# Performance work log

Hardware: AMD Instinct MI355X
Metric: run time of the kernel (lower is better)

## Reference

```python
import jax, jax.numpy as jnp
import numpy as np

DIM = 1024
HEADS = 16
HEAD_DIM = DIM // HEADS
HIDDEN = 4 * DIM
EPS = 1e-5


def layernorm(x, g, b):
    mu = jnp.mean(x, axis=-1, keepdims=True)
    var = jnp.var(x, axis=-1, keepdims=True)
    return (x - mu) * jax.lax.rsqrt(var + EPS) * g + b


def setup_inputs() -> dict:
    key = jax.random.key(0)
    ks = jax.random.split(key, 6)
    B, N = 4, 1024
    s = lambda fan_in: 1.0 / np.sqrt(fan_in)
    return {
        "x": jax.random.normal(ks[0], (B, N, DIM), jnp.float32),
        "ln1_g": jnp.ones((DIM,), jnp.float32),
        "ln1_b": jnp.zeros((DIM,), jnp.float32),
        "qkv_w": jax.random.normal(ks[1], (3 * DIM, DIM), jnp.float32) * s(DIM),
        "qkv_b": jnp.zeros((3 * DIM,), jnp.float32),
        "proj_w": jax.random.normal(ks[2], (DIM, DIM), jnp.float32) * s(DIM),
        "proj_b": jnp.zeros((DIM,), jnp.float32),
        "ln2_g": jnp.ones((DIM,), jnp.float32),
        "ln2_b": jnp.zeros((DIM,), jnp.float32),
        "fc1_w": jax.random.normal(ks[3], (HIDDEN, DIM), jnp.float32) * s(DIM),
        "fc1_b": jnp.zeros((HIDDEN,), jnp.float32),
        "fc2_w": jax.random.normal(ks[4], (DIM, HIDDEN), jnp.float32) * s(HIDDEN),
        "fc2_b": jnp.zeros((DIM,), jnp.float32),
    }


def reference(x, ln1_g, ln1_b, qkv_w, qkv_b, proj_w, proj_b,
              ln2_g, ln2_b, fc1_w, fc1_b, fc2_w, fc2_b):
    B, N, C = x.shape
    scale = HEAD_DIM ** -0.5

    # --- attention branch ---
    h = layernorm(x, ln1_g, ln1_b)
    qkv = h @ qkv_w.T + qkv_b                      # [B,N,3C]
    qkv = qkv.reshape(B, N, 3, HEADS, HEAD_DIM)
    q = qkv[:, :, 0].transpose(0, 2, 1, 3) * scale  # [B,H,N,D]
    k = qkv[:, :, 1].transpose(0, 2, 1, 3)
    v = qkv[:, :, 2].transpose(0, 2, 1, 3)
    attn = jax.nn.softmax(jnp.einsum('bhnd,bhmd->bhnm', q, k), axis=-1)
    o = jnp.einsum('bhnm,bhmd->bhnd', attn, v)      # [B,H,N,D]
    o = o.transpose(0, 2, 1, 3).reshape(B, N, C)
    x = x + (o @ proj_w.T + proj_b)

    # --- mlp branch ---
    h = layernorm(x, ln2_g, ln2_b)
    h = jax.nn.gelu(h @ fc1_w.T + fc1_b, approximate=False)
    x = x + (h @ fc2_w.T + fc2_b)
    return x
```

## Files before the change

kernel.cpp:

```cpp
#include <hip/hip_runtime.h>
#include <math.h>

#define DIM 1024
#define HEADS 16
#define HEAD_DIM 64
#define HIDDEN 4096
#define NSEQ 1024
#define BATCH 4
#define TOKENS (BATCH * NSEQ)
#define EPS 1e-5f

typedef __bf16 bf16;
typedef __bf16 bf16x4 __attribute__((ext_vector_type(4)));
typedef __bf16 bf16x8 __attribute__((ext_vector_type(8)));
typedef float f32x4 __attribute__((ext_vector_type(4)));

#define AS1 __attribute__((address_space(1)))
#define AS3 __attribute__((address_space(3)))

__global__ __launch_bounds__(256) void cvt4_kernel(const float* __restrict__ s0,
                                                   const float* __restrict__ s1,
                                                   const float* __restrict__ s2,
                                                   const float* __restrict__ s3,
                                                   bf16* __restrict__ d0,
                                                   bf16* __restrict__ d1,
                                                   bf16* __restrict__ d2,
                                                   bf16* __restrict__ d3) {
    size_t q = (size_t)blockIdx.x * 256 + threadIdx.x;
    const float* s;
    bf16* d;
    if (q < 786432) { s = s0; d = d0; }
    else if (q < 786432 + 262144) { q -= 786432; s = s1; d = d1; }
    else if (q < 786432 + 262144 + 1048576) { q -= 786432 + 262144; s = s2; d = d2; }
    else { q -= 786432 + 262144 + 1048576; s = s3; d = d3; }
    const float4 v = *(const float4*)(s + q * 4);
    bf16x4 o = {(bf16)v.x, (bf16)v.y, (bf16)v.z, (bf16)v.w};
    *(bf16x4*)(d + q * 4) = o;
}

__global__ __launch_bounds__(256) void ln_kernel(const float* __restrict__ x,
                                                 const float* __restrict__ g,
                                                 const float* __restrict__ b,
                                                 bf16* __restrict__ out) {
    const int t = blockIdx.x;
    const int tid = threadIdx.x;
    const float* row = x + (size_t)t * DIM;
    float v[4];
    float s1 = 0.f, s2 = 0.f;
#pragma unroll
    for (int i = 0; i < 4; i++) {
        v[i] = row[tid + i * 256];
        s1 += v[i];
        s2 += v[i] * v[i];
    }
    __shared__ float w1[4], w2[4];
#pragma unroll
    for (int off = 32; off > 0; off >>= 1) {
        s1 += __shfl_down(s1, off, 64);
        s2 += __shfl_down(s2, off, 64);
    }
    const int wave = tid >> 6;
    if ((tid & 63) == 0) { w1[wave] = s1; w2[wave] = s2; }
    __syncthreads();
    const float sum = w1[0] + w1[1] + w1[2] + w1[3];
    const float ssq = w2[0] + w2[1] + w2[2] + w2[3];
    const float mu = sum * (1.0f / DIM);
    const float var = ssq * (1.0f / DIM) - mu * mu;
    const float rstd = rsqrtf(var + EPS);
    bf16* orow = out + (size_t)t * DIM;
#pragma unroll
    for (int i = 0; i < 4; i++) {
        const int idx = tid + i * 256;
        orow[idx] = (bf16)((v[i] - mu) * rstd * g[idx] + b[idx]);
    }
}

#define ACT_NONE 0
#define ACT_GELU 1

template <int ACT, bool RES, bool OUT_BF16, bool VT, int SPLITK>
__global__ __launch_bounds__(256) void mfma_gemm(const bf16* __restrict__ A,
                                                 const bf16* __restrict__ W,
                                                 const float* __restrict__ bias,
                                                 const float* __restrict__ res,
                                                 void* __restrict__ Cout,
                                                 bf16* __restrict__ vTout,
                                                 int M, int N, int K) {
    __shared__ __align__(16) bf16 As[128 * 32];
    __shared__ __align__(16) bf16 Bs[128 * 32];

    const int tid = threadIdx.x;
    const int w = tid >> 6, lane = tid & 63;
    const int bm = blockIdx.y * 128, bn = blockIdx.x * 128;
    const int kseg = K / SPLITK;
    const int k0 = (SPLITK > 1) ? blockIdx.z * kseg : 0;

    const bf16* pa = A + (size_t)(bm + (tid >> 2)) * K + k0 + (tid & 3) * 8;
    const bf16* pb = W + (size_t)(bn + (tid >> 2)) * K + k0 + (tid & 3) * 8;
    const size_t rowskip = (size_t)64 * K;
    char* ldsA = (char*)As + (w << 10);
    char* ldsB = (char*)Bs + (w << 10);

    const int wm = (w & 1) * 64, wn = (w >> 1) * 64;
    const int fm = lane & 15, fk = (lane >> 4) * 8;
    const bf16* aoff = As + (wm + fm) * 32 + fk;
    const bf16* boff = Bs + (wn + fm) * 32 + fk;

    f32x4 acc[4][4] = {};

    for (int kk = 0; kk < kseg; kk += 32) {
        __builtin_amdgcn_global_load_lds((const AS1 void*)pa, (AS3 void*)ldsA, 16, 0, 0);
        __builtin_amdgcn_global_load_lds((const AS1 void*)(pa + rowskip), (AS3 void*)(ldsA + 4096), 16, 0, 0);
        __builtin_amdgcn_global_load_lds((const AS1 void*)pb, (AS3 void*)ldsB, 16, 0, 0);
        __builtin_amdgcn_global_load_lds((const AS1 void*)(pb + rowskip), (AS3 void*)(ldsB + 4096), 16, 0, 0);
        pa += 32; pb += 32;
        __syncthreads();

        bf16x8 af[4], bfr[4];
#pragma unroll
        for (int t = 0; t < 4; t++) af[t] = *(const bf16x8*)(aoff + t * 16 * 32);
#pragma unroll
        for (int t = 0; t < 4; t++) bfr[t] = *(const bf16x8*)(boff + t * 16 * 32);
#pragma unroll
        for (int mt = 0; mt < 4; mt++)
#pragma unroll
            for (int nt = 0; nt < 4; nt++)
                acc[mt][nt] = __builtin_amdgcn_mfma_f32_16x16x32_bf16(af[mt], bfr[nt], acc[mt][nt], 0, 0, 0);
        __syncthreads();
    }

    const int cn = bn + wn + fm;
    const int rm = bm + wm + (lane >> 4) * 4;
    float bv[4];
#pragma unroll
    for (int nt = 0; nt < 4; nt++)
        bv[nt] = (SPLITK > 1 && blockIdx.z != 0) ? 0.f : bias[cn + nt * 16];

    if (SPLITK > 1) {
        float* outp = (float*)Cout;
#pragma unroll
        for (int mt = 0; mt < 4; mt++) {
#pragma unroll
            for (int r = 0; r < 4; r++) {
                const size_t rowoff = (size_t)(rm + mt * 16 + r) * N;
#pragma unroll
                for (int nt = 0; nt < 4; nt++)
                    atomicAdd(outp + rowoff + cn + nt * 16, acc[mt][nt][r] + bv[nt]);
            }
        }
        return;
    }

    if (VT && bn >= 2048) {
        const int dg0 = cn - 2048;
#pragma unroll
        for (int mt = 0; mt < 4; mt++) {
            const int mrow = rm + mt * 16;
            const int bI = mrow >> 10, j0 = mrow & 1023;
#pragma unroll
            for (int nt = 0; nt < 4; nt++) {
                const int dg = dg0 + nt * 16;
                bf16x4 v4 = {(bf16)(acc[mt][nt][0] + bv[nt]), (bf16)(acc[mt][nt][1] + bv[nt]),
                             (bf16)(acc[mt][nt][2] + bv[nt]), (bf16)(acc[mt][nt][3] + bv[nt])};
                *(bf16x4*)(vTout + ((size_t)(bI * 1024 + dg)) * 1024 + j0) = v4;
            }
        }
        return;
    }

#pragma unroll
    for (int mt = 0; mt < 4; mt++) {
#pragma unroll
        for (int r = 0; r < 4; r++) {
            const size_t rowoff = (size_t)(rm + mt * 16 + r) * N;
#pragma unroll
            for (int nt = 0; nt < 4; nt++) {
                float val = acc[mt][nt][r] + bv[nt];
                if (ACT == ACT_GELU) val = 0.5f * val * (1.0f + erff(val * 0.70710678118654752f));
                if (RES) val += res[rowoff + cn + nt * 16];
                if (OUT_BF16) ((bf16*)Cout)[rowoff + cn + nt * 16] = (bf16)val;
                else          ((float*)Cout)[rowoff + cn + nt * 16] = val;
            }
        }
    }
}

__global__ __launch_bounds__(256) void fattn_mfma(const bf16* __restrict__ qkv,
                                                  const bf16* __restrict__ vT,
                                                  bf16* __restrict__ out) {
    __shared__ __align__(16) bf16 Ks[64 * 64];
    __shared__ __align__(16) bf16 Vt[64 * 64];
    __shared__ __align__(16) bf16 Ps[64 * 68];

    const int bid = blockIdx.x;
    const int qt = bid & 15;
    const int h = (bid >> 4) & 15;
    const int b = bid >> 8;
    const int tid = threadIdx.x;
    const int w = tid >> 6, lane = tid & 63;
    const int li = lane & 15, g = lane >> 4;

    bf16x8 aQ[2];
    {
        const size_t tok = (size_t)b * NSEQ + qt * 64 + w * 16 + li;
#pragma unroll
        for (int ks = 0; ks < 2; ks++)
            aQ[ks] = *(const bf16x8*)(qkv + tok * (3 * DIM) + h * HEAD_DIM + g * 8 + 32 * ks);
    }

    float mrun[4] = {-INFINITY, -INFINITY, -INFINITY, -INFINITY};
    float lrun[4] = {0.f, 0.f, 0.f, 0.f};
    f32x4 o[4] = {};

    const int idx0 = w * 128 + lane;
    const int idx1 = idx0 + 64;
    const int jl0 = idx0 >> 3, c0 = (idx0 & 7) ^ (jl0 & 7);
    const int jl1 = idx1 >> 3, c1 = (idx1 & 7) ^ (jl1 & 7);
    bf16* ldsK0 = Ks + (size_t)(w * 128) * 8;
    bf16* ldsK1 = Ks + (size_t)(w * 128 + 64) * 8;
    bf16* ldsV0 = Vt + (size_t)(w * 128) * 8;
    bf16* ldsV1 = Vt + (size_t)(w * 128 + 64) * 8;
    const bf16* kbase = qkv + (size_t)b * NSEQ * (3 * DIM) + DIM + h * HEAD_DIM;
    const bf16* vbase = vT + ((size_t)b * DIM + h * HEAD_DIM) * NSEQ;

    for (int k0 = 0; k0 < NSEQ; k0 += 64) {
        __syncthreads();
        __builtin_amdgcn_global_load_lds((const AS1 void*)(kbase + (size_t)(k0 + jl0) * (3 * DIM) + c0 * 8),
                                         (AS3 void*)ldsK0, 16, 0, 0);
        __builtin_amdgcn_global_load_lds((const AS1 void*)(kbase + (size_t)(k0 + jl1) * (3 * DIM) + c1 * 8),
                                         (AS3 void*)ldsK1, 16, 0, 0);
        __builtin_amdgcn_global_load_lds((const AS1 void*)(vbase + (size_t)jl0 * NSEQ + k0 + c0 * 8),
                                         (AS3 void*)ldsV0, 16, 0, 0);
        __builtin_amdgcn_global_load_lds((const AS1 void*)(vbase + (size_t)jl1 * NSEQ + k0 + c1 * 8),
                                         (AS3 void*)ldsV1, 16, 0, 0);
        __syncthreads();

        f32x4 s[4] = {};
#pragma unroll
        for (int ks = 0; ks < 2; ks++) {
#pragma unroll
            for (int nt = 0; nt < 4; nt++) {
                const int j = li + 16 * nt;
                const int p = (g + 4 * ks) ^ (j & 7);
                bf16x8 bK = *(const bf16x8*)(Ks + j * 64 + p * 8);
                s[nt] = __builtin_amdgcn_mfma_f32_16x16x32_bf16(aQ[ks], bK, s[nt], 0, 0, 0);
            }
        }
#pragma unroll
        for (int nt = 0; nt < 4; nt++) s[nt] *= 0.125f;

        float m4[4], rs[4], alpha[4];
#pragma unroll
        for (int r = 0; r < 4; r++)
            m4[r] = fmaxf(fmaxf(s[0][r], s[1][r]), fmaxf(s[2][r], s[3][r]));
#pragma unroll
        for (int mask = 1; mask < 16; mask <<= 1)
#pragma unroll
            for (int r = 0; r < 4; r++) m4[r] = fmaxf(m4[r], __shfl_xor(m4[r], mask, 64));
#pragma unroll
        for (int r = 0; r < 4; r++) {
            const float mn = fmaxf(mrun[r], m4[r]);
            alpha[r] = __expf(mrun[r] - mn);
            mrun[r] = mn;
        }
#pragma unroll
        for (int r = 0; r < 4; r++) rs[r] = 0.f;
#pragma unroll
        for (int nt = 0; nt < 4; nt++) {
#pragma unroll
            for (int r = 0; r < 4; r++) {
                const float p = __expf(s[nt][r] - mrun[r]);
                rs[r] += p;
                Ps[(w * 16 + g * 4 + r) * 68 + li + 16 * nt] = (bf16)p;
            }
        }
#pragma unroll
        for (int mask = 1; mask < 16; mask <<= 1)
#pragma unroll
            for (int r = 0; r < 4; r++) rs[r] += __shfl_xor(rs[r], mask, 64);
#pragma unroll
        for (int r = 0; r < 4; r++) lrun[r] = lrun[r] * alpha[r] + rs[r];
#pragma unroll
        for (int nt = 0; nt < 4; nt++)
#pragma unroll
            for (int r = 0; r < 4; r++) o[nt][r] *= alpha[r];

        bf16x8 aP[2];
#pragma unroll
        for (int ks = 0; ks < 2; ks++) {
            const int off = (w * 16 + li) * 68 + g * 8 + 32 * ks;
            bf16x4 lo = *(const bf16x4*)(Ps + off);
            bf16x4 hi = *(const bf16x4*)(Ps + off + 4);
            aP[ks] = bf16x8{lo[0], lo[1], lo[2], lo[3], hi[0], hi[1], hi[2], hi[3]};
        }
#pragma unroll
        for (int ks = 0; ks < 2; ks++) {
#pragma unroll
            for (int nt = 0; nt < 4; nt++) {
                const int d = li + 16 * nt;
                const int p = (g + 4 * ks) ^ (d & 7);
                bf16x8 bV = *(const bf16x8*)(Vt + d * 64 + p * 8);
                o[nt] = __builtin_amdgcn_mfma_f32_16x16x32_bf16(aP[ks], bV, o[nt], 0, 0, 0);
            }
        }
    }

    float linv[4];
#pragma unroll
    for (int r = 0; r < 4; r++) linv[r] = 1.0f / lrun[r];
    const size_t tok0 = (size_t)b * NSEQ + qt * 64 + w * 16 + g * 4;
#pragma unroll
    for (int r = 0; r < 4; r++) {
#pragma unroll
        for (int nt = 0; nt < 4; nt++)
            out[(tok0 + r) * DIM + h * HEAD_DIM + 16 * nt + li] = (bf16)(o[nt][r] * linv[r]);
    }
}

extern "C" void kernel_launch(void* const* d_in, const int* in_sizes, int n_in,
                              void* d_out, int out_size, void* d_ws, size_t ws_size,
                              hipStream_t stream) {
    const float* x      = (const float*)d_in[0];
    const float* ln1_g  = (const float*)d_in[1];
    const float* ln1_b  = (const float*)d_in[2];
    const float* qkv_w  = (const float*)d_in[3];
    const float* qkv_b  = (const float*)d_in[4];
    const float* proj_w = (const float*)d_in[5];
    const float* proj_b = (const float*)d_in[6];
    const float* ln2_g  = (const float*)d_in[7];
    const float* ln2_b  = (const float*)d_in[8];
    const float* fc1_w  = (const float*)d_in[9];
    const float* fc1_b  = (const float*)d_in[10];
    const float* fc2_w  = (const float*)d_in[11];
    const float* fc2_b  = (const float*)d_in[12];
    float* out = (float*)d_out;

    char* p = (char*)d_ws;
    bf16*  h_bf    = (bf16*)p;  p += (size_t)TOKENS * DIM * 2;
    bf16*  attn_bf = (bf16*)p;  p += (size_t)TOKENS * DIM * 2;
    bf16*  ffn_bf  = (bf16*)p;  p += (size_t)TOKENS * HIDDEN * 2;
    bf16*  qkv_bf  = (bf16*)p;  p += (size_t)TOKENS * 3 * DIM * 2;
    bf16*  vT_bf   = (bf16*)p;  p += (size_t)BATCH * DIM * NSEQ * 2;
    bf16*  wq_bf   = (bf16*)p;  p += (size_t)3 * DIM * DIM * 2;
    bf16*  wp_bf   = (bf16*)p;  p += (size_t)DIM * DIM * 2;
    bf16*  w1_bf   = (bf16*)p;  p += (size_t)HIDDEN * DIM * 2;
    bf16*  w2_bf   = (bf16*)p;  p += (size_t)DIM * HIDDEN * 2;

    cvt4_kernel<<<(3145728 + 1048576 + 4194304 + 4194304) / 1024, 256, 0, stream>>>(
        qkv_w, proj_w, fc1_w, fc2_w, wq_bf, wp_bf, w1_bf, w2_bf);

    ln_kernel<<<TOKENS, 256, 0, stream>>>(x, ln1_g, ln1_b, h_bf);
    mfma_gemm<ACT_NONE, false, true, true, 1><<<dim3(3 * DIM / 128, TOKENS / 128), 256, 0, stream>>>(
        h_bf, wq_bf, qkv_b, nullptr, qkv_bf, vT_bf, TOKENS, 3 * DIM, DIM);
    fattn_mfma<<<BATCH * HEADS * (NSEQ / 64), 256, 0, stream>>>(qkv_bf, vT_bf, attn_bf);
    hipMemcpyAsync(out, x, (size_t)TOKENS * DIM * sizeof(float), hipMemcpyDeviceToDevice, stream);
    mfma_gemm<ACT_NONE, false, false, false, 2><<<dim3(DIM / 128, TOKENS / 128, 2), 256, 0, stream>>>(
        attn_bf, wp_bf, proj_b, nullptr, out, nullptr, TOKENS, DIM, DIM);
    ln_kernel<<<TOKENS, 256, 0, stream>>>(out, ln2_g, ln2_b, h_bf);
    mfma_gemm<ACT_GELU, false, true, false, 1><<<dim3(HIDDEN / 128, TOKENS / 128), 256, 0, stream>>>(
        h_bf, w1_bf, fc1_b, nullptr, ffn_bf, nullptr, TOKENS, HIDDEN, DIM);
    mfma_gemm<ACT_NONE, false, false, false, 2><<<dim3(DIM / 128, TOKENS / 128, 2), 256, 0, stream>>>(
        ffn_bf, w2_bf, fc2_b, nullptr, out, nullptr, TOKENS, DIM, HIDDEN);
}
```

Before: 414.7 us.

## Double-buffer GEMM LDS tiles, fuse weight cast with LN1, raise split-K to four

The GEMM main loop now double-buffers its LDS tiles, issuing the global-to-LDS load for the next K slice before computing the current one, with a single barrier per iteration. The weight-cast kernel and the first layernorm are merged into one launch. The residual copy of x is replaced by a memset, with the z=0 split adding the residual inside the atomic epilogue. Both split-K GEMMs go from 2 to 4 splits. These changes aim to hide load latency, cut launch and copy overhead, and add parallelism, at the cost of more LDS per block and more atomic traffic.

```diff
diff --git a/kernel.cpp b/kernel.cpp
--- a/kernel.cpp
+++ b/kernel.cpp
@@ -18,7 +18,14 @@
 #define AS1 __attribute__((address_space(1)))
 #define AS3 __attribute__((address_space(3)))
 
-__global__ __launch_bounds__(256) void cvt4_kernel(const float* __restrict__ s0,
+#define CVT_QUADS 3145728
+#define CVT_BLOCKS 12288
+
+__global__ __launch_bounds__(256) void prep_kernel(const float* __restrict__ x,
+                                                   const float* __restrict__ g,
+                                                   const float* __restrict__ bb,
+                                                   bf16* __restrict__ h,
+                                                   const float* __restrict__ s0,
                                                    const float* __restrict__ s1,
                                                    const float* __restrict__ s2,
                                                    const float* __restrict__ s3,
@@ -26,16 +33,51 @@
                                                    bf16* __restrict__ d1,
                                                    bf16* __restrict__ d2,
                                                    bf16* __restrict__ d3) {
-    size_t q = (size_t)blockIdx.x * 256 + threadIdx.x;
-    const float* s;
-    bf16* d;
-    if (q < 786432) { s = s0; d = d0; }
-    else if (q < 786432 + 262144) { q -= 786432; s = s1; d = d1; }
-    else if (q < 786432 + 262144 + 1048576) { q -= 786432 + 262144; s = s2; d = d2; }
-    else { q -= 786432 + 262144 + 1048576; s = s3; d = d3; }
-    const float4 v = *(const float4*)(s + q * 4);
-    bf16x4 o = {(bf16)v.x, (bf16)v.y, (bf16)v.z, (bf16)v.w};
-    *(bf16x4*)(d + q * 4) = o;
+    const int blk = blockIdx.x;
+    const int tid = threadIdx.x;
+    if (blk < CVT_BLOCKS) {
+        size_t q = (size_t)blk * 256 + tid;
+        const float* s;
+        bf16* d;
+        if (q < 786432) { s = s0; d = d0; }
+        else if (q < 786432 + 262144) { q -= 786432; s = s1; d = d1; }
+        else if (q < 786432 + 262144 + 1048576) { q -= 786432 + 262144; s = s2; d = d2; }
+        else { q -= 786432 + 262144 + 1048576; s = s3; d = d3; }
+        const float4 v = *(const float4*)(s + q * 4);
+        bf16x4 o = {(bf16)v.x, (bf16)v.y, (bf16)v.z, (bf16)v.w};
+        *(bf16x4*)(d + q * 4) = o;
+        return;
+    }
+    const int t = blk - CVT_BLOCKS;
+    const float* row = x + (size_t)t * DIM;
+    float v[4];
+    float s1v = 0.f, s2v = 0.f;
+#pragma unroll
+    for (int i = 0; i < 4; i++) {
+        v[i] = row[tid + i * 256];
+        s1v += v[i];
+        s2v += v[i] * v[i];
+    }
+    __shared__ float w1[4], w2[4];
+#pragma unroll
+    for (int off = 32; off > 0; off >>= 1) {
+        s1v += __shfl_down(s1v, off, 64);
+        s2v += __shfl_down(s2v, off, 64);
+    }
+    const int wave = tid >> 6;
+    if ((tid & 63) == 0) { w1[wave] = s1v; w2[wave] = s2v; }
+    __syncthreads();
+    const float sum = w1[0] + w1[1] + w1[2] + w1[3];
+    const float ssq = w2[0] + w2[1] + w2[2] + w2[3];
+    const float mu = sum * (1.0f / DIM);
+    const float var = ssq * (1.0f / DIM) - mu * mu;
+    const float rstd = rsqrtf(var + EPS);
+    bf16* orow = h + (size_t)t * DIM;
+#pragma unroll
+    for (int i = 0; i < 4; i++) {
+        const int idx = tid + i * 256;
+        orow[idx] = (bf16)((v[i] - mu) * rstd * g[idx] + bb[idx]);
+    }
 }
 
 __global__ __launch_bounds__(256) void ln_kernel(const float* __restrict__ x,
@@ -86,8 +128,8 @@
                                                  void* __restrict__ Cout,
                                                  bf16* __restrict__ vTout,
                                                  int M, int N, int K) {
-    __shared__ __align__(16) bf16 As[128 * 32];
-    __shared__ __align__(16) bf16 Bs[128 * 32];
+    __shared__ __align__(16) bf16 As[2][128 * 32];
+    __shared__ __align__(16) bf16 Bs[2][128 * 32];
 
     const int tid = threadIdx.x;
     const int w = tid >> 6, lane = tid & 63;
@@ -98,35 +140,48 @@
     const bf16* pa = A + (size_t)(bm + (tid >> 2)) * K + k0 + (tid & 3) * 8;
     const bf16* pb = W + (size_t)(bn + (tid >> 2)) * K + k0 + (tid & 3) * 8;
     const size_t rowskip = (size_t)64 * K;
-    char* ldsA = (char*)As + (w << 10);
-    char* ldsB = (char*)Bs + (w << 10);
 
     const int wm = (w & 1) * 64, wn = (w >> 1) * 64;
     const int fm = lane & 15, fk = (lane >> 4) * 8;
-    const bf16* aoff = As + (wm + fm) * 32 + fk;
-    const bf16* boff = Bs + (wn + fm) * 32 + fk;
+    const int foffA = (wm + fm) * 32 + fk;
+    const int foffB = (wn + fm) * 32 + fk;
 
     f32x4 acc[4][4] = {};
 
+    {
+        char* lA = (char*)As[0] + (w << 10);
+        char* lB = (char*)Bs[0] + (w << 10);
+        __builtin_amdgcn_global_load_lds((const AS1 void*)pa, (AS3 void*)lA, 16, 0, 0);
+        __builtin_amdgcn_global_load_lds((const AS1 void*)(pa + rowskip), (AS3 void*)(lA + 4096), 16, 0, 0);
+        __builtin_amdgcn_global_load_lds((const AS1 void*)pb, (AS3 void*)lB, 16, 0, 0);
+        __builtin_amdgcn_global_load_lds((const AS1 void*)(pb + rowskip), (AS3 void*)(lB + 4096), 16, 0, 0);
+        pa += 32; pb += 32;
+    }
+
     for (int kk = 0; kk < kseg; kk += 32) {
-        __builtin_amdgcn_global_load_lds((const AS1 void*)pa, (AS3 void*)ldsA, 16, 0, 0);
-        __builtin_amdgcn_global_load_lds((const AS1 void*)(pa + rowskip), (AS3 void*)(ldsA + 4096), 16, 0, 0);
-        __builtin_amdgcn_global_load_lds((const AS1 void*)pb, (AS3 void*)ldsB, 16, 0, 0);
-        __builtin_amdgcn_global_load_lds((const AS1 void*)(pb + rowskip), (AS3 void*)(ldsB + 4096), 16, 0, 0);
-        pa += 32; pb += 32;
+        const int p = (kk >> 5) & 1;
         __syncthreads();
-
+        if (kk + 32 < kseg) {
+            char* lA = (char*)As[p ^ 1] + (w << 10);
+            char* lB = (char*)Bs[p ^ 1] + (w << 10);
+            __builtin_amdgcn_global_load_lds((const AS1 void*)pa, (AS3 void*)lA, 16, 0, 0);
+            __builtin_amdgcn_global_load_lds((const AS1 void*)(pa + rowskip), (AS3 void*)(lA + 4096), 16, 0, 0);
+            __builtin_amdgcn_global_load_lds((const AS1 void*)pb, (AS3 void*)lB, 16, 0, 0);
+            __builtin_amdgcn_global_load_lds((const AS1 void*)(pb + rowskip), (AS3 void*)(lB + 4096), 16, 0, 0);
+            pa += 32; pb += 32;
+        }
+        const bf16* ab = As[p] + foffA;
+        const bf16* bb = Bs[p] + foffB;
         bf16x8 af[4], bfr[4];
 #pragma unroll
-        for (int t = 0; t < 4; t++) af[t] = *(const bf16x8*)(aoff + t * 16 * 32);
-#pragma unroll
-        for (int t = 0; t < 4; t++) bfr[t] = *(const bf16x8*)(boff + t * 16 * 32);
+        for (int t = 0; t < 4; t++) af[t] = *(const bf16x8*)(ab + t * 16 * 32);
+#pragma unroll
+        for (int t = 0; t < 4; t++) bfr[t] = *(const bf16x8*)(bb + t * 16 * 32);
 #pragma unroll
         for (int mt = 0; mt < 4; mt++)
 #pragma unroll
             for (int nt = 0; nt < 4; nt++)
                 acc[mt][nt] = __builtin_amdgcn_mfma_f32_16x16x32_bf16(af[mt], bfr[nt], acc[mt][nt], 0, 0, 0);
-        __syncthreads();
     }
 
     const int cn = bn + wn + fm;
@@ -138,14 +193,18 @@
 
     if (SPLITK > 1) {
         float* outp = (float*)Cout;
+        const bool z0 = (blockIdx.z == 0);
 #pragma unroll
         for (int mt = 0; mt < 4; mt++) {
 #pragma unroll
             for (int r = 0; r < 4; r++) {
                 const size_t rowoff = (size_t)(rm + mt * 16 + r) * N;
 #pragma unroll
-                for (int nt = 0; nt < 4; nt++)
-                    atomicAdd(outp + rowoff + cn + nt * 16, acc[mt][nt][r] + bv[nt]);
+                for (int nt = 0; nt < 4; nt++) {
+                    float val = acc[mt][nt][r] + bv[nt];
+                    if (RES && z0) val += res[rowoff + cn + nt * 16];
+                    atomicAdd(outp + rowoff + cn + nt * 16, val);
+                }
             }
         }
         return;
@@ -346,19 +405,17 @@
     bf16*  w1_bf   = (bf16*)p;  p += (size_t)HIDDEN * DIM * 2;
     bf16*  w2_bf   = (bf16*)p;  p += (size_t)DIM * HIDDEN * 2;
 
-    cvt4_kernel<<<(3145728 + 1048576 + 4194304 + 4194304) / 1024, 256, 0, stream>>>(
-        qkv_w, proj_w, fc1_w, fc2_w, wq_bf, wp_bf, w1_bf, w2_bf);
-
-    ln_kernel<<<TOKENS, 256, 0, stream>>>(x, ln1_g, ln1_b, h_bf);
+    prep_kernel<<<CVT_BLOCKS + TOKENS, 256, 0, stream>>>(
+        x, ln1_g, ln1_b, h_bf, qkv_w, proj_w, fc1_w, fc2_w, wq_bf, wp_bf, w1_bf, w2_bf);
     mfma_gemm<ACT_NONE, false, true, true, 1><<<dim3(3 * DIM / 128, TOKENS / 128), 256, 0, stream>>>(
         h_bf, wq_bf, qkv_b, nullptr, qkv_bf, vT_bf, TOKENS, 3 * DIM, DIM);
     fattn_mfma<<<BATCH * HEADS * (NSEQ / 64), 256, 0, stream>>>(qkv_bf, vT_bf, attn_bf);
-    hipMemcpyAsync(out, x, (size_t)TOKENS * DIM * sizeof(float), hipMemcpyDeviceToDevice, stream);
-    mfma_gemm<ACT_NONE, false, false, false, 2><<<dim3(DIM / 128, TOKENS / 128, 2), 256, 0, stream>>>(
-        attn_bf, wp_bf, proj_b, nullptr, out, nullptr, TOKENS, DIM, DIM);
+    hipMemsetAsync(out, 0, (size_t)TOKENS * DIM * sizeof(float), stream);
+    mfma_gemm<ACT_NONE, true, false, false, 4><<<dim3(DIM / 128, TOKENS / 128, 4), 256, 0, stream>>>(
+        attn_bf, wp_bf, proj_b, x, out, nullptr, TOKENS, DIM, DIM);
     ln_kernel<<<TOKENS, 256, 0, stream>>>(out, ln2_g, ln2_b, h_bf);
     mfma_gemm<ACT_GELU, false, true, false, 1><<<dim3(HIDDEN / 128, TOKENS / 128), 256, 0, stream>>>(
         h_bf, w1_bf, fc1_b, nullptr, ffn_bf, nullptr, TOKENS, HIDDEN, DIM);
-    mfma_gemm<ACT_NONE, false, false, false, 2><<<dim3(DIM / 128, TOKENS / 128, 2), 256, 0, stream>>>(
+    mfma_gemm<ACT_NONE, false, false, false, 4><<<dim3(DIM / 128, TOKENS / 128, 4), 256, 0, stream>>>(
         ffn_bf, w2_bf, fc2_b, nullptr, out, nullptr, TOKENS, DIM, HIDDEN);
 }
```

Measured after the change: 450.0 us. 1.09x slower.
